# Kernel tuning notes

Hardware: AMD Instinct MI355X
Metric: run time of the kernel (lower is better)

## Reference

```python
import jax, jax.numpy as jnp
import numpy as np

N_POINTS = 1440   # number of detector angles (thetas)
N_INT = 4000      # trapezoid integration samples along each ray
N_GRID = 4096     # SoS field is (N_GRID, N_GRID)
GRID_LO, GRID_HI = -0.06, 0.06
R_BODY = 0.05
V0 = 1500.0


def setup_inputs() -> dict:
    key = jax.random.key(0)
    k1, k2, k3 = jax.random.split(key, 3)
    # query point strictly inside the body circle (r < R_body)
    x = jnp.float32(0.012)
    y = jnp.float32(-0.007)
    # speed-of-sound field ~ water SoS with heterogeneity, strictly positive
    SoS = (1480.0 + 40.0 * jax.random.uniform(k3, (N_GRID, N_GRID))).astype(jnp.float32)
    thetas = jnp.linspace(0.0, 2.0 * jnp.pi, N_POINTS, dtype=jnp.float32).reshape(-1, 1)
    steps = jnp.linspace(0.0, 1.0, N_INT, dtype=jnp.float32).reshape(1, -1)
    x_vec = jnp.linspace(GRID_LO, GRID_HI, N_GRID, dtype=jnp.float32)
    dx = x_vec[1] - x_vec[0]
    return {
        "x": x, "y": y, "SoS": SoS,
        "thetas": thetas, "steps": steps,
        "x0": x_vec[0], "y0": x_vec[0], "dx": dx, "dy": dx,
        "R_body": jnp.float32(R_BODY), "v0": jnp.float32(V0),
    }


def reference(x, y, SoS, thetas, steps, x0, y0, dx, dy, R_body, v0):
    # polar coords of query point; note torch code uses atan2(x, y)
    r = jnp.sqrt(x * x + y * y)
    phi = jnp.arctan2(x, y)
    s = r * jnp.sin(thetas - phi)                      # (P,1)
    arg = jnp.maximum(R_body * R_body - s * s, 0.0)    # shared, >0 when r<R_body
    sqrt_arg = jnp.sqrt(arg)
    l_in = sqrt_arg + r * jnp.cos(thetas - phi)
    l_out = 2.0 * sqrt_arg * (jnp.cos(phi - thetas) >= 0.0).astype(sqrt_arg.dtype)
    l = jnp.where(r < R_body, l_in, l_out)             # (P,1) chord lengths

    xs = l * steps                                     # (P,N) arc-length samples
    px = x - xs * jnp.sin(thetas)                      # (P,N) sample positions
    py = y - xs * jnp.cos(thetas)
    x_index = jnp.round((px - x0) / dx).astype(jnp.int32)
    y_index = jnp.round((py - y0) / dy).astype(jnp.int32)
    # gather: negative row index (-y_index) wraps from the end, as in torch/numpy
    vals = 1.0 - v0 / SoS[-y_index, x_index]           # (P,N)
    # trapezoid over non-uniformly labeled x = l*steps (uniform per row)
    dseg = jnp.diff(xs, axis=1)                        # (P,N-1)
    wf = jnp.sum(0.5 * (vals[:, :-1] + vals[:, 1:]) * dseg, axis=1)
    return thetas.reshape(-1), wf
```

## Files before the change

kernel.cpp:

```cpp
#include <hip/hip_runtime.h>

#define N_POINTS 1440
#define N_INT    4000
#define N_GRID   4096
#define BLOCK    256
#define MAIN_ITERS (N_INT / BLOCK)
#define REMAIN     (N_INT - MAIN_ITERS * BLOCK)

__global__ __launch_bounds__(256) void wavefront_sos_kernel(
    const float* __restrict__ xp,
    const float* __restrict__ yp,
    const float* __restrict__ SoS,
    const float* __restrict__ thetas,
    const float* __restrict__ x0p,
    const float* __restrict__ y0p,
    const float* __restrict__ dxp,
    const float* __restrict__ dyp,
    const float* __restrict__ Rp,
    const float* __restrict__ v0p,
    float* __restrict__ out)
{
    const int b = blockIdx.x;
    const int p = (b & 7) * (N_POINTS / 8) + (b >> 3);

    const float x  = xp[0];
    const float y  = yp[0];
    const float x0 = x0p[0];
    const float y0 = y0p[0];
    const float dx = dxp[0];
    const float dy = dyp[0];
    const float Rb = Rp[0];
    const float v0 = v0p[0];

    const float theta = thetas[p];

    const float r   = sqrtf(x * x + y * y);
    const float phi = atan2f(x, y);
    const float st  = sinf(theta);
    const float ct  = cosf(theta);

    const float s     = r * sinf(theta - phi);
    const float arg   = fmaxf(Rb * Rb - s * s, 0.0f);
    const float sq    = sqrtf(arg);
    const float l_in  = sq + r * cosf(theta - phi);
    const float l_out = 2.0f * sq * (cosf(phi - theta) >= 0.0f ? 1.0f : 0.0f);
    const float l     = (r < Rb) ? l_in : l_out;

    const float ds = 1.0f / 3999.0f;
    const float Ax = (x - x0) / dx;
    const float Bx = l * st / dx;
    const float Ay = (y - y0) / dy;
    const float By = l * ct / dy;

    const float s_base = (float)threadIdx.x * ds;
    const float fx0 = fmaf(-Bx, s_base, Ax);
    const float fy0 = fmaf(-By, s_base, Ay);
    const float nBxd = -Bx * (256.0f * ds);
    const float nByd = -By * (256.0f * ds);

    float acc = 0.0f;

#define SAMPLE(itf, vdst)                                            \
    {                                                                \
        const float fx = fmaf((itf), nBxd, fx0);                     \
        const float fy = fmaf((itf), nByd, fy0);                     \
        const int xi = (int)rintf(fx);                               \
        const int yi = (int)rintf(fy);                               \
        const int idx = ((N_GRID - yi) << 12) + xi;                  \
        const float sosv = SoS[idx];                                 \
        vdst = fmaf(-v0, __builtin_amdgcn_rcpf(sosv), 1.0f);         \
    }

#pragma unroll
    for (int it = 0; it < MAIN_ITERS; ++it) {
        float v;
        SAMPLE((float)it, v);
        if (it == 0 && threadIdx.x == 0) v *= 0.5f;
        acc += v;
    }
    if (threadIdx.x < REMAIN) {
        float v;
        SAMPLE((float)MAIN_ITERS, v);
        if (threadIdx.x == REMAIN - 1) v *= 0.5f;
        acc += v;
    }
#undef SAMPLE

    for (int off = 32; off > 0; off >>= 1)
        acc += __shfl_down(acc, off, 64);

    __shared__ float wave_sums[4];
    const int lane = threadIdx.x & 63;
    const int wave = threadIdx.x >> 6;
    if (lane == 0) wave_sums[wave] = acc;
    __syncthreads();

    if (threadIdx.x == 0) {
        const float total = wave_sums[0] + wave_sums[1] + wave_sums[2] + wave_sums[3];
        const float wf = l * ds * total;
        out[p] = theta;
        out[N_POINTS + p] = wf;
    }
}

extern "C" void kernel_launch(void* const* d_in, const int* in_sizes, int n_in,
                              void* d_out, int out_size, void* d_ws, size_t ws_size,
                              hipStream_t stream) {
    (void)in_sizes; (void)n_in; (void)out_size; (void)d_ws; (void)ws_size;

    const float* xp     = (const float*)d_in[0];
    const float* yp     = (const float*)d_in[1];
    const float* SoS    = (const float*)d_in[2];
    const float* thetas = (const float*)d_in[3];
    const float* x0p    = (const float*)d_in[5];
    const float* y0p    = (const float*)d_in[6];
    const float* dxp    = (const float*)d_in[7];
    const float* dyp    = (const float*)d_in[8];
    const float* Rp     = (const float*)d_in[9];
    const float* v0p    = (const float*)d_in[10];

    float* out = (float*)d_out;

    wavefront_sos_kernel<<<N_POINTS, BLOCK, 0, stream>>>(
        xp, yp, SoS, thetas, x0p, y0p, dxp, dyp, Rp, v0p, out);
}
```

Measured before the change: 119.2 us.

## Interleave 8 rays per block and split rays into segments with combine pass

Each block now handles 8 adjacent rays, with lanes interleaved by ray and each ray split into 16 segments across blocks. Neighbouring thetas sample nearby grid cells, so the intent is to improve cache locality of the scattered SoS gathers and to raise the number of blocks for better load balance. Partial sums go to workspace and a second small kernel reduces them and computes the final chord scaling. This adds a second launch and a workspace round trip. Adjacent lanes also now hit different rays, which can reduce coalescing within a wavefront.

```diff
diff --git a/kernel.cpp b/kernel.cpp
--- a/kernel.cpp
+++ b/kernel.cpp
@@ -4,10 +4,16 @@
 #define N_INT    4000
 #define N_GRID   4096
 #define BLOCK    256
-#define MAIN_ITERS (N_INT / BLOCK)
-#define REMAIN     (N_INT - MAIN_ITERS * BLOCK)
 
-__global__ __launch_bounds__(256) void wavefront_sos_kernel(
+#define NSEG     16
+#define SEG_LEN  (N_INT / NSEG)
+#define RPC      8
+#define NCLUST   (N_POINTS / RPC)
+#define QS       (BLOCK / RPC)
+#define FULL_ITS (SEG_LEN / QS)
+#define REM_Q    (SEG_LEN - FULL_ITS * QS)
+
+__global__ __launch_bounds__(BLOCK, 8) void wavefront_partial_kernel(
     const float* __restrict__ xp,
     const float* __restrict__ yp,
     const float* __restrict__ SoS,
@@ -18,10 +24,16 @@
     const float* __restrict__ dyp,
     const float* __restrict__ Rp,
     const float* __restrict__ v0p,
-    float* __restrict__ out)
+    float* __restrict__ ws)
 {
     const int b = blockIdx.x;
-    const int p = (b & 7) * (N_POINTS / 8) + (b >> 3);
+    const int c = b >> 4;
+    const int S = b & 15;
+    const int t = threadIdx.x;
+    const int r = t & 7;
+    const int q = t >> 3;
+
+    const int p = c * RPC + r;
 
     const float x  = xp[0];
     const float y  = yp[0];
@@ -34,17 +46,17 @@
 
     const float theta = thetas[p];
 
-    const float r   = sqrtf(x * x + y * y);
+    const float rr  = sqrtf(x * x + y * y);
     const float phi = atan2f(x, y);
     const float st  = sinf(theta);
     const float ct  = cosf(theta);
 
-    const float s     = r * sinf(theta - phi);
-    const float arg   = fmaxf(Rb * Rb - s * s, 0.0f);
+    const float sv    = rr * sinf(theta - phi);
+    const float arg   = fmaxf(Rb * Rb - sv * sv, 0.0f);
     const float sq    = sqrtf(arg);
-    const float l_in  = sq + r * cosf(theta - phi);
+    const float l_in  = sq + rr * cosf(theta - phi);
     const float l_out = 2.0f * sq * (cosf(phi - theta) >= 0.0f ? 1.0f : 0.0f);
-    const float l     = (r < Rb) ? l_in : l_out;
+    const float l     = (rr < Rb) ? l_in : l_out;
 
     const float ds = 1.0f / 3999.0f;
     const float Ax = (x - x0) / dx;
@@ -52,13 +64,14 @@
     const float Ay = (y - y0) / dy;
     const float By = l * ct / dy;
 
-    const float s_base = (float)threadIdx.x * ds;
-    const float fx0 = fmaf(-Bx, s_base, Ax);
-    const float fy0 = fmaf(-By, s_base, Ay);
-    const float nBxd = -Bx * (256.0f * ds);
-    const float nByd = -By * (256.0f * ds);
+    const int   jb     = S * SEG_LEN + q;
+    const float s_base = (float)jb * ds;
+    const float fx0  = fmaf(-Bx, s_base, Ax);
+    const float fy0  = fmaf(-By, s_base, Ay);
+    const float nBxd = -Bx * ((float)QS * ds);
+    const float nByd = -By * ((float)QS * ds);
 
-    float acc = 0.0f;
+    float acc;
 
 #define SAMPLE(itf, vdst)                                            \
     {                                                                \
@@ -71,42 +84,69 @@
         vdst = fmaf(-v0, __builtin_amdgcn_rcpf(sosv), 1.0f);         \
     }
 
+    { float v; SAMPLE(0.0f, v); if (S == 0 && q == 0) v *= 0.5f; acc = v; }
 #pragma unroll
-    for (int it = 0; it < MAIN_ITERS; ++it) {
-        float v;
-        SAMPLE((float)it, v);
-        if (it == 0 && threadIdx.x == 0) v *= 0.5f;
-        acc += v;
+    for (int it = 1; it < FULL_ITS; ++it) {
+        float v; SAMPLE((float)it, v); acc += v;
     }
-    if (threadIdx.x < REMAIN) {
-        float v;
-        SAMPLE((float)MAIN_ITERS, v);
-        if (threadIdx.x == REMAIN - 1) v *= 0.5f;
+    if (q < REM_Q) {
+        float v; SAMPLE((float)FULL_ITS, v);
+        if (S == NSEG - 1 && q == REM_Q - 1) v *= 0.5f;
         acc += v;
     }
 #undef SAMPLE
 
-    for (int off = 32; off > 0; off >>= 1)
-        acc += __shfl_down(acc, off, 64);
+    acc += __shfl_xor(acc, 8, 64);
+    acc += __shfl_xor(acc, 16, 64);
+    acc += __shfl_xor(acc, 32, 64);
 
-    __shared__ float wave_sums[4];
-    const int lane = threadIdx.x & 63;
-    const int wave = threadIdx.x >> 6;
-    if (lane == 0) wave_sums[wave] = acc;
+    __shared__ float wsum[4][8];
+    if ((t & 63) < 8) wsum[t >> 6][r] = acc;
     __syncthreads();
+    if (t < 8) {
+        const float tot = (wsum[0][t] + wsum[1][t]) + (wsum[2][t] + wsum[3][t]);
+        ws[(c * RPC + t) * NSEG + S] = tot;
+    }
+}
 
-    if (threadIdx.x == 0) {
-        const float total = wave_sums[0] + wave_sums[1] + wave_sums[2] + wave_sums[3];
-        const float wf = l * ds * total;
-        out[p] = theta;
-        out[N_POINTS + p] = wf;
-    }
+__global__ __launch_bounds__(BLOCK) void wavefront_combine_kernel(
+    const float* __restrict__ xp,
+    const float* __restrict__ yp,
+    const float* __restrict__ thetas,
+    const float* __restrict__ Rp,
+    const float* __restrict__ ws,
+    float* __restrict__ out)
+{
+    const int p = blockIdx.x * BLOCK + threadIdx.x;
+    if (p >= N_POINTS) return;
+
+    const float x  = xp[0];
+    const float y  = yp[0];
+    const float Rb = Rp[0];
+    const float theta = thetas[p];
+
+    const float rr  = sqrtf(x * x + y * y);
+    const float phi = atan2f(x, y);
+    const float sv    = rr * sinf(theta - phi);
+    const float arg   = fmaxf(Rb * Rb - sv * sv, 0.0f);
+    const float sq    = sqrtf(arg);
+    const float l_in  = sq + rr * cosf(theta - phi);
+    const float l_out = 2.0f * sq * (cosf(phi - theta) >= 0.0f ? 1.0f : 0.0f);
+    const float l     = (rr < Rb) ? l_in : l_out;
+
+    const float4* w4 = (const float4*)(ws + p * NSEG);
+    const float4 a = w4[0], b4 = w4[1], c4 = w4[2], d4 = w4[3];
+    const float tot = (((a.x + a.y) + (a.z + a.w)) + ((b4.x + b4.y) + (b4.z + b4.w)))
+                    + (((c4.x + c4.y) + (c4.z + c4.w)) + ((d4.x + d4.y) + (d4.z + d4.w)));
+
+    out[p] = theta;
+    out[N_POINTS + p] = l * (1.0f / 3999.0f) * tot;
 }
 
 extern "C" void kernel_launch(void* const* d_in, const int* in_sizes, int n_in,
                               void* d_out, int out_size, void* d_ws, size_t ws_size,
                               hipStream_t stream) {
-    (void)in_sizes; (void)n_in; (void)out_size; (void)d_ws; (void)ws_size;
+    (void)in_sizes; (void)n_in; (void)out_size; (void)ws_size;
 
     const float* xp     = (const float*)d_in[0];
     const float* yp     = (const float*)d_in[1];
@@ -119,8 +159,11 @@
     const float* Rp     = (const float*)d_in[9];
     const float* v0p    = (const float*)d_in[10];
 
+    float* ws  = (float*)d_ws;
     float* out = (float*)d_out;
 
-    wavefront_sos_kernel<<<N_POINTS, BLOCK, 0, stream>>>(
-        xp, yp, SoS, thetas, x0p, y0p, dxp, dyp, Rp, v0p, out);
+    wavefront_partial_kernel<<<NCLUST * NSEG, BLOCK, 0, stream>>>(
+        xp, yp, SoS, thetas, x0p, y0p, dxp, dyp, Rp, v0p, ws);
+    wavefront_combine_kernel<<<(N_POINTS + BLOCK - 1) / BLOCK, BLOCK, 0, stream>>>(
+        xp, yp, thetas, Rp, ws, out);
 }
```

Result: no change. 117.3 us (-1.6%).
